# Kernel optimization log

Hardware: AMD Instinct MI355X
Metric: run time of the kernel (lower is better)

## Reference

```python
import jax, jax.numpy as jnp
import numpy as np

N, E, F_IN, HEADS, C_HEAD, HID, B, NCLS = 20000, 320000, 128, 2, 256, 512, 64, 38
EL = E + N  # edges with self-loops appended


def _bn(x, g, b, eps=1e-5):
    mu = jnp.mean(x, 0)
    var = jnp.mean((x - mu) ** 2, 0)
    return g * (x - mu) * jax.lax.rsqrt(var + eps) + b


def _gcn(x, W, b, src, dst):
    # src/dst already include self-loops; symmetric deg^-1/2 normalization (PyG GCNConv)
    h = x @ W                                             # [N, HID]
    deg = jax.ops.segment_sum(jnp.ones(EL, x.dtype), dst, N)
    norm = jax.lax.rsqrt(jnp.maximum(deg, 1.0))
    coef = norm[src] * norm[dst]                          # [EL]
    agg = jax.ops.segment_sum(h[src] * coef[:, None], dst, N)
    return agg + b


def _gat(x, W, a_src, a_dst, b, src, dst):
    # PyG GATConv, heads=2, concat: alpha = softmax_dst(leaky_relu(a_s.h_src + a_d.h_dst))
    h = (x @ W).reshape(N, HEADS, C_HEAD)
    as_n = jnp.sum(h * a_src, -1)                         # [N, HEADS]
    ad_n = jnp.sum(h * a_dst, -1)
    e = jax.nn.leaky_relu(as_n[src] + ad_n[dst], 0.2)     # [EL, HEADS]
    m = jax.ops.segment_max(e, dst, N)
    ex = jnp.exp(e - m[dst])
    s = jax.ops.segment_sum(ex, dst, N)
    alpha = ex / s[dst]                                   # [EL, HEADS]
    out = jax.ops.segment_sum(h[src] * alpha[:, :, None], dst, N)
    return out.reshape(N, HEADS * C_HEAD) + b


def setup_inputs() -> dict:
    key = jax.random.key(0)
    ks = jax.random.split(key, 40)
    x = jax.random.normal(ks[0], (N, F_IN), jnp.float32)
    edge_index = jax.random.randint(ks[1], (2, E), 0, N, jnp.int32)
    batch = jnp.sort(jax.random.randint(ks[2], (N,), 0, B, jnp.int32))

    def lin(k, fi, fo):
        bound = np.sqrt(6.0 / fi)
        return jax.random.uniform(k, (fi, fo), jnp.float32, -bound, bound)

    d = dict(x=x, edge_index=edge_index, batch=batch)
    # feature transform
    d['ft_W'] = lin(ks[3], F_IN, HID); d['ft_b'] = jnp.zeros(HID)
    d['ft_g'] = jnp.ones(HID); d['ft_be'] = jnp.zeros(HID)
    # GCN block
    d['gcn1_W'] = lin(ks[4], HID, HID); d['gcn1_b'] = jnp.zeros(HID)
    d['gbn1_g'] = jnp.ones(HID); d['gbn1_b'] = jnp.zeros(HID)
    d['gcn2_W'] = lin(ks[5], HID, HID); d['gcn2_b'] = jnp.zeros(HID)
    d['gbn2_g'] = jnp.ones(HID); d['gbn2_b'] = jnp.zeros(HID)
    # GAT block
    abound = np.sqrt(6.0 / HEADS)
    d['gat1_W'] = lin(ks[6], HID, HID)
    d['gat1_as'] = jax.random.uniform(ks[7], (HEADS, C_HEAD), jnp.float32, -abound, abound)
    d['gat1_ad'] = jax.random.uniform(ks[8], (HEADS, C_HEAD), jnp.float32, -abound, abound)
    d['gat1_b'] = jnp.zeros(HID)
    d['abn1_g'] = jnp.ones(HID); d['abn1_b'] = jnp.zeros(HID)
    d['gat2_W'] = lin(ks[9], HID, HID)
    d['gat2_as'] = jax.random.uniform(ks[10], (HEADS, C_HEAD), jnp.float32, -abound, abound)
    d['gat2_ad'] = jax.random.uniform(ks[11], (HEADS, C_HEAD), jnp.float32, -abound, abound)
    d['gat2_b'] = jnp.zeros(HID)
    d['abn2_g'] = jnp.ones(HID); d['abn2_b'] = jnp.zeros(HID)
    # classifier
    d['fc1_W'] = lin(ks[12], 2 * HID, HID); d['fc1_b'] = jnp.zeros(HID)
    d['cbn1_g'] = jnp.ones(HID); d['cbn1_b'] = jnp.zeros(HID)
    d['fc2_W'] = lin(ks[13], HID, HID // 2); d['fc2_b'] = jnp.zeros(HID // 2)
    d['cbn2_g'] = jnp.ones(HID // 2); d['cbn2_b'] = jnp.zeros(HID // 2)
    d['out_W'] = lin(ks[14], HID // 2, NCLS); d['out_b'] = jnp.zeros(NCLS)
    return d


def reference(x, edge_index, batch,
              ft_W, ft_b, ft_g, ft_be,
              gcn1_W, gcn1_b, gbn1_g, gbn1_b, gcn2_W, gcn2_b, gbn2_g, gbn2_b,
              gat1_W, gat1_as, gat1_ad, gat1_b, abn1_g, abn1_b,
              gat2_W, gat2_as, gat2_ad, gat2_b, abn2_g, abn2_b,
              fc1_W, fc1_b, cbn1_g, cbn1_b, fc2_W, fc2_b, cbn2_g, cbn2_b,
              out_W, out_b):
    loop = jnp.arange(N, dtype=edge_index.dtype)
    src = jnp.concatenate([edge_index[0], loop])
    dst = jnp.concatenate([edge_index[1], loop])

    # feature transform: Linear -> BN -> LeakyReLU(0.2)
    h = jax.nn.leaky_relu(_bn(x @ ft_W + ft_b, ft_g, ft_be), 0.2)
    # GCN block
    h = jax.nn.elu(_bn(_gcn(h, gcn1_W, gcn1_b, src, dst), gbn1_g, gbn1_b))
    h = jax.nn.elu(_bn(_gcn(h, gcn2_W, gcn2_b, src, dst), gbn2_g, gbn2_b))
    # GAT block
    h = jax.nn.elu(_bn(_gat(h, gat1_W, gat1_as, gat1_ad, gat1_b, src, dst), abn1_g, abn1_b))
    h = jax.nn.elu(_bn(_gat(h, gat2_W, gat2_as, gat2_ad, gat2_b, src, dst), abn2_g, abn2_b))
    # global mean+max pool over graphs
    cnt = jax.ops.segment_sum(jnp.ones(N, h.dtype), batch, B)
    mean_p = jax.ops.segment_sum(h, batch, B) / jnp.maximum(cnt, 1.0)[:, None]
    max_p = jax.ops.segment_max(h, batch, B)
    p = jnp.concatenate([mean_p, max_p], axis=1)           # [B, 1024]
    # classifier: fc1 -> bn -> fc2 -> bn -> leaky_relu -> out
    z = _bn(p @ fc1_W + fc1_b, cbn1_g, cbn1_b)
    z = _bn(z @ fc2_W + fc2_b, cbn2_g, cbn2_b)
    z = jax.nn.leaky_relu(z, 0.2)
    return z @ out_W + out_b                                # [B, NCLS]
```

## Files before the change

### kernel.cpp

```cpp
#include <hip/hip_runtime.h>

#define N_NODES 20000
#define N_EDGES 320000
#define EDG_ALL (N_EDGES + N_NODES)
#define F_IN 128
#define HID 512
#define NB 64
#define NCLS 38
#define M_PAD2 20480
#define ROW_BLKS 160
#define NBLK_SCAN ((N_NODES + 255) / 256)
#define BN_ROWS 16
#define BN_GRID ((N_NODES + BN_ROWS - 1) / BN_ROWS)
#define NPART 64
#define POOL_SPLIT 4

typedef short bf16x8 __attribute__((ext_vector_type(8)));
typedef float f32x4 __attribute__((ext_vector_type(4)));
typedef _Float16 f16;
typedef _Float16 f16x8 __attribute__((ext_vector_type(8)));

__device__ inline unsigned short f2bf(float f) {
  union { float f; unsigned u; } v; v.f = f;
  unsigned r = v.u + 0x7FFF + ((v.u >> 16) & 1);
  return (unsigned short)(r >> 16);
}

__device__ inline void split2(float f, unsigned short& h, unsigned short& l) {
  unsigned short hh = f2bf(f);
  union { unsigned u; float f; } vh; vh.u = ((unsigned)hh) << 16;
  h = hh;
  l = f2bf(f - vh.f);
}

__device__ inline void gload16(const void* g, void* l) {
  __builtin_amdgcn_global_load_lds(
      (const __attribute__((address_space(1))) unsigned int*)g,
      (__attribute__((address_space(3))) unsigned int*)l, 16, 0, 0);
}


__global__ void deg_count(const int* __restrict__ ei, int* __restrict__ deg) {
  int e = blockIdx.x * blockDim.x + threadIdx.x;
  if (e >= EDG_ALL) return;
  int d = (e < N_EDGES) ? ei[N_EDGES + e] : (e - N_EDGES);
  atomicAdd(&deg[d], 1);
}

__global__ void scan_p1(const int* __restrict__ deg, int* __restrict__ bsum) {
  __shared__ int sh[256];
  int b = blockIdx.x, t = threadIdx.x, i = b * 256 + t;
  sh[t] = (i < N_NODES) ? deg[i] : 0;
  __syncthreads();
  for (int o = 128; o > 0; o >>= 1) {
    if (t < o) sh[t] += sh[t + o];
    __syncthreads();
  }
  if (t == 0) bsum[b] = sh[0];
}

__global__ void scan_p2(const int* __restrict__ bsum, int* __restrict__ boff) {
  __shared__ int sh[128];
  int t = threadIdx.x;
  sh[t] = (t < NBLK_SCAN) ? bsum[t] : 0;
  __syncthreads();
  for (int o = 1; o < 128; o <<= 1) {
    int v = (t >= o) ? sh[t - o] : 0;
    __syncthreads();
    sh[t] += v;
    __syncthreads();
  }
  boff[t] = (t == 0) ? 0 : sh[t - 1];
}

__global__ void scan_p3(const int* __restrict__ deg, const int* __restrict__ boff,
                        int* __restrict__ row_ptr) {
  __shared__ int sh[256];
  int b = blockIdx.x, t = threadIdx.x, i = b * 256 + t;
  sh[t] = (i < N_NODES) ? deg[i] : 0;
  __syncthreads();
  for (int o = 1; o < 256; o <<= 1) {
    int v = (t >= o) ? sh[t - o] : 0;
    __syncthreads();
    sh[t] += v;
    __syncthreads();
  }
  if (i < N_NODES) row_ptr[i + 1] = boff[b] + sh[t];
  if (i == 0) row_ptr[0] = 0;
}

__global__ void compute_norm(const int* __restrict__ deg, float* __restrict__ norm) {
  int i = blockIdx.x * blockDim.x + threadIdx.x;
  if (i >= N_NODES) return;
  norm[i] = rsqrtf(fmaxf((float)deg[i], 1.f));
}

__global__ void fill_csr(const int* __restrict__ ei, int* __restrict__ cursor,
                         int* __restrict__ csr_src) {
  int e = blockIdx.x * blockDim.x + threadIdx.x;
  if (e >= EDG_ALL) return;
  int s, d;
  if (e < N_EDGES) { s = ei[e]; d = ei[N_EDGES + e]; }
  else { s = d = e - N_EDGES; }
  int pos = atomicAdd(&cursor[d], 1);
  csr_src[pos] = s;
}


__global__ void conv_split4(const float* __restrict__ in, unsigned short* __restrict__ hi,
                            unsigned short* __restrict__ lo, int n4) {
  int i = blockIdx.x * blockDim.x + threadIdx.x;
  if (i >= n4) return;
  float4 v = ((const float4*)in)[i];
  ushort4 h, l;
  split2(v.x, h.x, l.x); split2(v.y, h.y, l.y);
  split2(v.z, h.z, l.z); split2(v.w, h.w, l.w);
  ((ushort4*)hi)[i] = h;
  ((ushort4*)lo)[i] = l;
}

__global__ __launch_bounds__(256) void wtrans_split(const float* __restrict__ W,
                                                    unsigned short* __restrict__ WTh,
                                                    unsigned short* __restrict__ WTl,
                                                    int K, int N) {
  __shared__ float sh[32][33];
  int k0 = blockIdx.y * 32, n0 = blockIdx.x * 32;
  int r = threadIdx.x >> 5, c = threadIdx.x & 31;
#pragma unroll
  for (int i = 0; i < 4; ++i)
    sh[r + 8 * i][c] = W[(size_t)(k0 + r + 8 * i) * N + n0 + c];
  __syncthreads();
#pragma unroll
  for (int i = 0; i < 4; ++i) {
    unsigned short h, l;
    split2(sh[c][r + 8 * i], h, l);
    WTh[(size_t)(n0 + r + 8 * i) * K + k0 + c] = h;
    WTl[(size_t)(n0 + r + 8 * i) * K + k0 + c] = l;
  }
}

__global__ __launch_bounds__(256) void ftrans(const float* __restrict__ W,
                                              float* __restrict__ WT, int K, int N) {
  __shared__ float sh[32][33];
  int k0 = blockIdx.y * 32, n0 = blockIdx.x * 32;
  int r = threadIdx.x >> 5, c = threadIdx.x & 31;
#pragma unroll
  for (int i = 0; i < 4; ++i) {
    int k = k0 + r + 8 * i, n = n0 + c;
    sh[r + 8 * i][c] = (k < K && n < N) ? W[(size_t)k * N + n] : 0.f;
  }
  __syncthreads();
#pragma unroll
  for (int i = 0; i < 4; ++i) {
    int n = n0 + r + 8 * i, k = k0 + c;
    if (n < N && k < K) WT[(size_t)n * K + k] = sh[c][r + 8 * i];
  }
}


template <int K, typename OT>
__global__ __launch_bounds__(256) void mm_split(const unsigned short* __restrict__ Ah,
                                                const unsigned short* __restrict__ Al,
                                                const unsigned short* __restrict__ Bh,
                                                const unsigned short* __restrict__ Bl,
                                                const float* __restrict__ bias,
                                                OT* __restrict__ C) {
  __shared__ unsigned short AsH[4096], AsL[4096], BsH[4096], BsL[4096];
  const int t = threadIdx.x;
  const int wid = t >> 6, l = t & 63;
  const int bid = blockIdx.x;
  const int g = bid >> 5, w = bid & 31;
  const int row0 = (g * 8 + (w & 7)) * 128;
  const int col0 = (w >> 3) * 128;
  const int wm = wid >> 1, wn = wid & 1;

  f32x4 acc[4][4];
#pragma unroll
  for (int m = 0; m < 4; ++m)
#pragma unroll
    for (int n = 0; n < 4; ++n)
#pragma unroll
      for (int q = 0; q < 4; ++q) acc[m][n][q] = 0.f;

  const size_t aoff = (size_t)(row0 + wid * 32 + (l >> 2)) * K + (l & 3) * 8;
  const size_t boff = (size_t)(col0 + wid * 32 + (l >> 2)) * K + (l & 3) * 8;
  const unsigned short* gAh0 = Ah + aoff; const unsigned short* gAh1 = gAh0 + (size_t)16 * K;
  const unsigned short* gAl0 = Al + aoff; const unsigned short* gAl1 = gAl0 + (size_t)16 * K;
  const unsigned short* gBh0 = Bh + boff; const unsigned short* gBh1 = gBh0 + (size_t)16 * K;
  const unsigned short* gBl0 = Bl + boff; const unsigned short* gBl1 = gBl0 + (size_t)16 * K;
  unsigned short* lAh0 = &AsH[(wid * 2 + 0) * 512];
  unsigned short* lAh1 = &AsH[(wid * 2 + 1) * 512];
  unsigned short* lAl0 = &AsL[(wid * 2 + 0) * 512];
  unsigned short* lAl1 = &AsL[(wid * 2 + 1) * 512];
  unsigned short* lBh0 = &BsH[(wid * 2 + 0) * 512];
  unsigned short* lBh1 = &BsH[(wid * 2 + 1) * 512];
  unsigned short* lBl0 = &BsL[(wid * 2 + 0) * 512];
  unsigned short* lBl1 = &BsL[(wid * 2 + 1) * 512];

  const int lr = l & 15, kq = (l >> 4) * 8;

  for (int kt = 0; kt < K / 32; ++kt) {
    const int ko = kt * 32;
    gload16(gAh0 + ko, lAh0);
    gload16(gAh1 + ko, lAh1);
    gload16(gAl0 + ko, lAl0);
    gload16(gAl1 + ko, lAl1);
    gload16(gBh0 + ko, lBh0);
    gload16(gBh1 + ko, lBh1);
    gload16(gBl0 + ko, lBl0);
    gload16(gBl1 + ko, lBl1);
    __syncthreads();
    bf16x8 ah[4], al[4], bh[4], bl[4];
#pragma unroll
    for (int m = 0; m < 4; ++m) {
      int ro = (wm * 64 + m * 16 + lr) * 32 + kq;
      ah[m] = *(const bf16x8*)&AsH[ro];
      al[m] = *(const bf16x8*)&AsL[ro];
    }
#pragma unroll
    for (int n = 0; n < 4; ++n) {
      int ro = (wn * 64 + n * 16 + lr) * 32 + kq;
      bh[n] = *(const bf16x8*)&BsH[ro];
      bl[n] = *(const bf16x8*)&BsL[ro];
    }
#pragma unroll
    for (int m = 0; m < 4; ++m)
#pragma unroll
      for (int n = 0; n < 4; ++n) {
        acc[m][n] = __builtin_amdgcn_mfma_f32_16x16x32_bf16(ah[m], bh[n], acc[m][n], 0, 0, 0);
        acc[m][n] = __builtin_amdgcn_mfma_f32_16x16x32_bf16(al[m], bh[n], acc[m][n], 0, 0, 0);
        acc[m][n] = __builtin_amdgcn_mfma_f32_16x16x32_bf16(ah[m], bl[n], acc[m][n], 0, 0, 0);
      }
    __syncthreads();
  }

  const int lg = l >> 4;
#pragma unroll
  for (int m = 0; m < 4; ++m) {
    int row = row0 + wm * 64 + m * 16 + lg * 4;
#pragma unroll
    for (int n = 0; n < 4; ++n) {
      int col = col0 + wn * 64 + n * 16 + lr;
      float bv = bias ? bias[col] : 0.f;
#pragma unroll
      for (int j = 0; j < 4; ++j)
        C[(size_t)(row + j) * HID + col] = (OT)(acc[m][n][j] + bv);
    }
  }
}


__global__ __launch_bounds__(256) void colstats(const float* __restrict__ X, int n,
                                                float* __restrict__ part) {
  int t = threadIdx.x;
  int r0 = blockIdx.x * BN_ROWS;
  int r1 = min(r0 + BN_ROWS, n);
  float s0 = 0, q0 = 0, s1 = 0, q1 = 0;
  const float2* X2 = (const float2*)X;
  for (int r = r0; r < r1; ++r) {
    float2 v = X2[(size_t)r * 256 + t];
    s0 += v.x; q0 += v.x * v.x;
    s1 += v.y; q1 += v.y * v.y;
  }
  float* pb = part + (size_t)(blockIdx.x & (NPART - 1)) * 1024;
  atomicAdd(&pb[2 * t], s0);
  atomicAdd(&pb[2 * t + 1], s1);
  atomicAdd(&pb[HID + 2 * t], q0);
  atomicAdd(&pb[HID + 2 * t + 1], q1);
}

__global__ __launch_bounds__(256) void stats_comb(const float* __restrict__ part,
                                                  float* __restrict__ stats) {
  int j = blockIdx.x * 256 + threadIdx.x;
  float s = 0.f;
#pragma unroll 8
  for (int k = 0; k < NPART; ++k) s += part[(size_t)k * 1024 + j];
  stats[j] = s;
}

__global__ __launch_bounds__(256) void bn_act(float* __restrict__ X, int n,
                                              const float* __restrict__ stats,
                                              const float* __restrict__ g,
                                              const float* __restrict__ b, int act,
                                              unsigned short* __restrict__ hio,
                                              unsigned short* __restrict__ loo,
                                              int writeX) {
  int t = threadIdx.x;
  int r0 = blockIdx.x * BN_ROWS;
  int r1 = min(r0 + BN_ROWS, n);
  float invn = 1.f / (float)n;
  float mu0 = stats[2 * t] * invn, mu1 = stats[2 * t + 1] * invn;
  float v0 = stats[HID + 2 * t] * invn - mu0 * mu0;
  float v1 = stats[HID + 2 * t + 1] * invn - mu1 * mu1;
  float2 gg = ((const float2*)g)[t];
  float2 bb = ((const float2*)b)[t];
  float sc0 = gg.x * rsqrtf(v0 + 1e-5f);
  float sc1 = gg.y * rsqrtf(v1 + 1e-5f);
  float2* X2 = (float2*)X;
  ushort2* H2 = (ushort2*)hio;
  ushort2* L2p = (ushort2*)loo;
  for (int r = r0; r < r1; ++r) {
    float2 xv = X2[(size_t)r * 256 + t];
    float y0 = sc0 * (xv.x - mu0) + bb.x;
    float y1 = sc1 * (xv.y - mu1) + bb.y;
    if (act == 1) {
      y0 = y0 > 0.f ? y0 : 0.2f * y0;
      y1 = y1 > 0.f ? y1 : 0.2f * y1;
    } else {
      y0 = y0 > 0.f ? y0 : expm1f(y0);
      y1 = y1 > 0.f ? y1 : expm1f(y1);
    }
    unsigned short h0, l0, h1, l1;
    split2(y0, h0, l0);
    split2(y1, h1, l1);
    ushort2 hh; hh.x = h0; hh.y = h1;
    ushort2 ll; ll.x = l0; ll.y = l1;
    H2[(size_t)r * 256 + t] = hh;
    L2p[(size_t)r * 256 + t] = ll;
    if (writeX) {
      float2 yv; yv.x = y0; yv.y = y1;
      X2[(size_t)r * 256 + t] = yv;
    }
  }
}


__global__ __launch_bounds__(256) void gcn_agg_w(
    const f16* __restrict__ h, const int* __restrict__ row_ptr,
    const int* __restrict__ csr_src, const float* __restrict__ norm,
    const float* __restrict__ bias, float* __restrict__ out) {
  int node = blockIdx.x * 4 + (threadIdx.x >> 6);
  int l = threadIdx.x & 63;
  int beg = row_ptr[node], end = row_ptr[node + 1];
  float ni = norm[node];
  const f16x8* h8 = (const f16x8*)h;
  float acc[8] = {};
  int e = beg;
  for (; e + 4 <= end; e += 4) {
    int s0 = csr_src[e], s1 = csr_src[e + 1], s2 = csr_src[e + 2], s3 = csr_src[e + 3];
    float c0 = norm[s0] * ni, c1 = norm[s1] * ni, c2 = norm[s2] * ni, c3 = norm[s3] * ni;
    f16x8 v0 = h8[(size_t)s0 * 64 + l];
    f16x8 v1 = h8[(size_t)s1 * 64 + l];
    f16x8 v2 = h8[(size_t)s2 * 64 + l];
    f16x8 v3 = h8[(size_t)s3 * 64 + l];
#pragma unroll
    for (int k = 0; k < 8; ++k)
      acc[k] += c0 * (float)v0[k] + c1 * (float)v1[k] + c2 * (float)v2[k] + c3 * (float)v3[k];
  }
  for (; e < end; ++e) {
    int s = csr_src[e];
    float c = norm[s] * ni;
    f16x8 v = h8[(size_t)s * 64 + l];
#pragma unroll
    for (int k = 0; k < 8; ++k) acc[k] += c * (float)v[k];
  }
  float4 b0 = ((const float4*)bias)[l * 2];
  float4 b1 = ((const float4*)bias)[l * 2 + 1];
  float4 o0, o1;
  o0.x = acc[0] + b0.x; o0.y = acc[1] + b0.y; o0.z = acc[2] + b0.z; o0.w = acc[3] + b0.w;
  o1.x = acc[4] + b1.x; o1.y = acc[5] + b1.y; o1.z = acc[6] + b1.z; o1.w = acc[7] + b1.w;
  ((float4*)out)[(size_t)node * 128 + l * 2] = o0;
  ((float4*)out)[(size_t)node * 128 + l * 2 + 1] = o1;
}


__device__ inline float wave_sum(float v) {
#pragma unroll
  for (int o = 32; o > 0; o >>= 1) v += __shfl_down(v, o);
  return v;
}

typedef _Float16 f16x2 __attribute__((ext_vector_type(2)));
__global__ __launch_bounds__(256) void gat_prep_h(
    const f16* __restrict__ h, const float* __restrict__ a_src,
    const float* __restrict__ a_dst, float* __restrict__ asn, float* __restrict__ adn) {
  int i = blockIdx.x;
  int t = threadIdx.x;
  f16x2 hv = ((const f16x2*)h)[(size_t)i * 256 + t];
  float2 as2 = ((const float2*)a_src)[t];
  float2 ad2 = ((const float2*)a_dst)[t];
  float h0 = (float)hv.x, h1 = (float)hv.y;
  float s = h0 * as2.x + h1 * as2.y;
  float d = h0 * ad2.x + h1 * ad2.y;
  s = wave_sum(s); d = wave_sum(d);
  __shared__ float red[4][2];
  int w = t >> 6;
  if ((t & 63) == 0) { red[w][0] = s; red[w][1] = d; }
  __syncthreads();
  if (t == 0) {
    asn[2 * i]     = red[0][0] + red[1][0];
    asn[2 * i + 1] = red[2][0] + red[3][0];
    adn[2 * i]     = red[0][1] + red[1][1];
    adn[2 * i + 1] = red[2][1] + red[3][1];
  }
}

__device__ inline float lrelu(float v) { return v > 0.f ? v : 0.2f * v; }

__global__ __launch_bounds__(256) void gat_agg_w(
    const f16* __restrict__ h, const int* __restrict__ row_ptr,
    const int* __restrict__ csr_src, const float* __restrict__ asn,
    const float* __restrict__ adn, const float* __restrict__ bias,
    float* __restrict__ out) {
  int node = blockIdx.x * 4 + (threadIdx.x >> 6);
  int l = threadIdx.x & 63;
  int beg = row_ptr[node], end = row_ptr[node + 1];
  float ad0 = adn[2 * node], ad1 = adn[2 * node + 1];

  float m0 = -3.4e38f, m1 = -3.4e38f;
  for (int e = beg + l; e < end; e += 64) {
    int s = csr_src[e];
    m0 = fmaxf(m0, lrelu(asn[2 * s] + ad0));
    m1 = fmaxf(m1, lrelu(asn[2 * s + 1] + ad1));
  }
#pragma unroll
  for (int o = 32; o > 0; o >>= 1) {
    m0 = fmaxf(m0, __shfl_down(m0, o));
    m1 = fmaxf(m1, __shfl_down(m1, o));
  }
  float M0 = __shfl(m0, 0);
  float M1 = __shfl(m1, 0);

  const f16x8* h8 = (const f16x8*)h;
  float acc[8] = {};
  float sw0 = 0.f, sw1 = 0.f;
  int e = beg;
  for (; e + 4 <= end; e += 4) {
    int s0 = csr_src[e], s1 = csr_src[e + 1], s2 = csr_src[e + 2], s3 = csr_src[e + 3];
    float w00 = expf(lrelu(asn[2 * s0] + ad0) - M0), w01 = expf(lrelu(asn[2 * s0 + 1] + ad1) - M1);
    float w10 = expf(lrelu(asn[2 * s1] + ad0) - M0), w11 = expf(lrelu(asn[2 * s1 + 1] + ad1) - M1);
    float w20 = expf(lrelu(asn[2 * s2] + ad0) - M0), w21 = expf(lrelu(asn[2 * s2 + 1] + ad1) - M1);
    float w30 = expf(lrelu(asn[2 * s3] + ad0) - M0), w31 = expf(lrelu(asn[2 * s3 + 1] + ad1) - M1);
    sw0 += w00 + w10 + w20 + w30;
    sw1 += w01 + w11 + w21 + w31;
    f16x8 v0 = h8[(size_t)s0 * 64 + l];
    f16x8 v1 = h8[(size_t)s1 * 64 + l];
    f16x8 v2 = h8[(size_t)s2 * 64 + l];
    f16x8 v3 = h8[(size_t)s3 * 64 + l];
    float u0 = (l < 32) ? w00 : w01;
    float u1 = (l < 32) ? w10 : w11;
    float u2 = (l < 32) ? w20 : w21;
    float u3 = (l < 32) ? w30 : w31;
#pragma unroll
    for (int k = 0; k < 8; ++k)
      acc[k] += u0 * (float)v0[k] + u1 * (float)v1[k] + u2 * (float)v2[k] + u3 * (float)v3[k];
  }
  for (; e < end; ++e) {
    int s = csr_src[e];
    float w0 = expf(lrelu(asn[2 * s] + ad0) - M0);
    float w1 = expf(lrelu(asn[2 * s + 1] + ad1) - M1);
    sw0 += w0; sw1 += w1;
    f16x8 v = h8[(size_t)s * 64 + l];
    float u = (l < 32) ? w0 : w1;
#pragma unroll
    for (int k = 0; k < 8; ++k) acc[k] += u * (float)v[k];
  }
  float iS = (l < 32) ? (1.f / sw0) : (1.f / sw1);
  float4 b0 = ((const float4*)bias)[l * 2];
  float4 b1 = ((const float4*)bias)[l * 2 + 1];
  float4 o0, o1;
  o0.x = acc[0] * iS + b0.x; o0.y = acc[1] * iS + b0.y;
  o0.z = acc[2] * iS + b0.z; o0.w = acc[3] * iS + b0.w;
  o1.x = acc[4] * iS + b1.x; o1.y = acc[5] * iS + b1.y;
  o1.z = acc[6] * iS + b1.z; o1.w = acc[7] * iS + b1.w;
  ((float4*)out)[(size_t)node * 128 + l * 2] = o0;
  ((float4*)out)[(size_t)node * 128 + l * 2 + 1] = o1;
}


__global__ void graph_starts(const int* __restrict__ batch, int* __restrict__ start) {
  int i = blockIdx.x * blockDim.x + threadIdx.x;
  if (i >= N_NODES) return;
  int b = batch[i];
  int bp = (i == 0) ? -1 : batch[i - 1];
  for (int g = bp + 1; g <= b; ++g) start[g] = i;
  if (i == N_NODES - 1) {
    for (int g = b + 1; g <= NB; ++g) start[g] = N_NODES;
  }
}

__global__ __launch_bounds__(512) void pool_part(const float* __restrict__ h,
                                                 const int* __restrict__ start,
                                                 float* __restrict__ pp_sum,
                                                 float* __restrict__ pp_max) {
  int b = blockIdx.x, ch = blockIdx.y, t = threadIdx.x;
  int s = start[b], e = start[b + 1];
  int len = e - s;
  int c0 = s + (len * ch) / POOL_SPLIT;
  int c1 = s + (len * (ch + 1)) / POOL_SPLIT;
  float sum = 0.f, mx = -3.4e38f;
  int r = c0;
  for (; r + 4 <= c1; r += 4) {
    float v0 = h[(size_t)(r + 0) * HID + t];
    float v1 = h[(size_t)(r + 1) * HID + t];
    float v2 = h[(size_t)(r + 2) * HID + t];
    float v3 = h[(size_t)(r + 3) * HID + t];
    sum += v0 + v1 + v2 + v3;
    mx = fmaxf(mx, fmaxf(fmaxf(v0, v1), fmaxf(v2, v3)));
  }
  for (; r < c1; ++r) {
    float v = h[(size_t)r * HID + t];
    sum += v; mx = fmaxf(mx, v);
  }
  pp_sum[((size_t)b * POOL_SPLIT + ch) * HID + t] = sum;
  pp_max[((size_t)b * POOL_SPLIT + ch) * HID + t] = mx;
}

__global__ __launch_bounds__(512) void pool_comb(const float* __restrict__ pp_sum,
                                                 const float* __restrict__ pp_max,
                                                 const int* __restrict__ start,
                                                 float* __restrict__ p) {
  int b = blockIdx.x, t = threadIdx.x;
  float sum = 0.f, mx = -3.4e38f;
#pragma unroll
  for (int ch = 0; ch < POOL_SPLIT; ++ch) {
    sum += pp_sum[((size_t)b * POOL_SPLIT + ch) * HID + t];
    mx = fmaxf(mx, pp_max[((size_t)b * POOL_SPLIT + ch) * HID + t]);
  }
  float cnt = (float)(start[b + 1] - start[b]);
  p[b * 1024 + t] = sum / fmaxf(cnt, 1.f);
  p[b * 1024 + 512 + t] = mx;
}


__global__ __launch_bounds__(256) void fc_wave(const float* __restrict__ A,
                                               const float* __restrict__ WT,
                                               const float* __restrict__ bias,
                                               float* __restrict__ C, int K, int Ncol) {
  int r = blockIdx.x;
  int wid = threadIdx.x >> 6, l = threadIdx.x & 63;
  int c = blockIdx.y * 4 + wid;
  if (c >= Ncol) return;
  const float* a = A + (size_t)r * K;
  const float* w = WT + (size_t)c * K;
  float s = 0.f;
  for (int k = l; k < K; k += 64) s += a[k] * w[k];
#pragma unroll
  for (int o = 32; o > 0; o >>= 1) s += __shfl_down(s, o);
  if (l == 0) C[(size_t)r * Ncol + c] = s + bias[c];
}

__global__ void bn_small(float* __restrict__ X, int R, int C,
                         const float* __restrict__ g, const float* __restrict__ b, int act) {
  int c = blockIdx.x * blockDim.x + threadIdx.x;
  if (c >= C) return;
  float s = 0.f, q = 0.f;
  for (int r = 0; r < R; ++r) {
    float v = X[r * C + c];
    s += v; q += v * v;
  }
  float mu = s / R;
  float var = q / R - mu * mu;
  float sc = g[c] * rsqrtf(var + 1e-5f);
  float bb = b[c];
  for (int r = 0; r < R; ++r) {
    float v = sc * (X[r * C + c] - mu) + bb;
    if (act == 1) v = v > 0.f ? v : 0.2f * v;
    X[r * C + c] = v;
  }
}


extern "C" void kernel_launch(void* const* d_in, const int* in_sizes, int n_in,
                              void* d_out, int out_size, void* d_ws, size_t ws_size,
                              hipStream_t stream) {
  const float* x      = (const float*)d_in[0];
  const int*   ei     = (const int*)d_in[1];
  const int*   batch  = (const int*)d_in[2];
  const float* ft_W   = (const float*)d_in[3];
  const float* ft_b   = (const float*)d_in[4];
  const float* ft_g   = (const float*)d_in[5];
  const float* ft_be  = (const float*)d_in[6];
  const float* gcn1_W = (const float*)d_in[7];
  const float* gcn1_b = (const float*)d_in[8];
  const float* gbn1_g = (const float*)d_in[9];
  const float* gbn1_b = (const float*)d_in[10];
  const float* gcn2_W = (const float*)d_in[11];
  const float* gcn2_b = (const float*)d_in[12];
  const float* gbn2_g = (const float*)d_in[13];
  const float* gbn2_b = (const float*)d_in[14];
  const float* gat1_W = (const float*)d_in[15];
  const float* gat1_as= (const float*)d_in[16];
  const float* gat1_ad= (const float*)d_in[17];
  const float* gat1_b = (const float*)d_in[18];
  const float* abn1_g = (const float*)d_in[19];
  const float* abn1_b = (const float*)d_in[20];
  const float* gat2_W = (const float*)d_in[21];
  const float* gat2_as= (const float*)d_in[22];
  const float* gat2_ad= (const float*)d_in[23];
  const float* gat2_b = (const float*)d_in[24];
  const float* abn2_g = (const float*)d_in[25];
  const float* abn2_b = (const float*)d_in[26];
  const float* fc1_W  = (const float*)d_in[27];
  const float* fc1_b  = (const float*)d_in[28];
  const float* cbn1_g = (const float*)d_in[29];
  const float* cbn1_b = (const float*)d_in[30];
  const float* fc2_W  = (const float*)d_in[31];
  const float* fc2_b  = (const float*)d_in[32];
  const float* cbn2_g = (const float*)d_in[33];
  const float* cbn2_b = (const float*)d_in[34];
  const float* out_W  = (const float*)d_in[35];
  const float* out_b  = (const float*)d_in[36];

  char* ws = (char*)d_ws;
  size_t off = 0;
  auto alloc = [&](size_t bytes) -> void* {
    void* p = ws + off;
    off = (off + bytes + 255) & ~(size_t)255;
    return p;
  };

  float* buf0 = (float*)alloc((size_t)M_PAD2 * HID * 4);
  float* buf1 = (float*)alloc((size_t)M_PAD2 * HID * 4);
  unsigned short* ahi = (unsigned short*)alloc((size_t)M_PAD2 * HID * 2);
  unsigned short* alo = (unsigned short*)alloc((size_t)M_PAD2 * HID * 2);
  unsigned short* wh_ft = (unsigned short*)alloc((size_t)HID * F_IN * 2);
  unsigned short* wl_ft = (unsigned short*)alloc((size_t)HID * F_IN * 2);
  unsigned short* wh_g1 = (unsigned short*)alloc((size_t)HID * HID * 2);
  unsigned short* wl_g1 = (unsigned short*)alloc((size_t)HID * HID * 2);
  unsigned short* wh_g2 = (unsigned short*)alloc((size_t)HID * HID * 2);
  unsigned short* wl_g2 = (unsigned short*)alloc((size_t)HID * HID * 2);
  unsigned short* wh_a1 = (unsigned short*)alloc((size_t)HID * HID * 2);
  unsigned short* wl_a1 = (unsigned short*)alloc((size_t)HID * HID * 2);
  unsigned short* wh_a2 = (unsigned short*)alloc((size_t)HID * HID * 2);
  unsigned short* wl_a2 = (unsigned short*)alloc((size_t)HID * HID * 2);
  float* fc1t = (float*)alloc((size_t)512 * 1024 * 4);
  float* fc2t = (float*)alloc((size_t)256 * 512 * 4);
  float* outt = (float*)alloc((size_t)NCLS * 256 * 4);
  int*   row_ptr = (int*)alloc((N_NODES + 1) * 4);
  int*   cursor  = (int*)alloc(N_NODES * 4);
  int*   deg     = (int*)alloc(N_NODES * 4);
  int*   csr_src = (int*)alloc(EDG_ALL * 4);
  float* norm    = (float*)alloc(N_NODES * 4);
  float* asn     = (float*)alloc(N_NODES * 2 * 4);
  float* adn     = (float*)alloc(N_NODES * 2 * 4);
  float* stats   = (float*)alloc(1024 * 4);
  float* spart   = (float*)alloc((size_t)NPART * 1024 * 4);
  int*   bsum    = (int*)alloc(128 * 4);
  int*   boff    = (int*)alloc(128 * 4);
  int*   start   = (int*)alloc((NB + 1) * 4);
  float* p       = (float*)alloc(NB * 1024 * 4);
  float* pp_sum  = (float*)alloc((size_t)NB * POOL_SPLIT * HID * 4);
  float* pp_max  = (float*)alloc((size_t)NB * POOL_SPLIT * HID * 4);
  float* z1      = (float*)alloc(NB * HID * 4);
  float* z2      = (float*)alloc(NB * 256 * 4);
  unsigned short* xhi = (unsigned short*)buf0;
  unsigned short* xlo = xhi + (size_t)M_PAD2 * F_IN;
  f16* hbuf = (f16*)buf1;

  const dim3 blk256(256);
  const dim3 mmGrid(ROW_BLKS * 4);
  const int aggGrid = N_NODES / 4;

#define BN_BLOCK(XBUF, G, B, ACT, WX)                                            \
  hipMemsetAsync(spart, 0, (size_t)NPART * 1024 * 4, stream);                    \
  colstats<<<BN_GRID, blk256, 0, stream>>>(XBUF, N_NODES, spart);                \
  stats_comb<<<4, blk256, 0, stream>>>(spart, stats);                            \
  bn_act<<<BN_GRID, blk256, 0, stream>>>(XBUF, N_NODES, stats, G, B, ACT, ahi, alo, WX);

  hipMemsetAsync(deg, 0, N_NODES * 4, stream);
  deg_count<<<(EDG_ALL + 255) / 256, blk256, 0, stream>>>(ei, deg);
  scan_p1<<<NBLK_SCAN, blk256, 0, stream>>>(deg, bsum);
  scan_p2<<<1, 128, 0, stream>>>(bsum, boff);
  scan_p3<<<NBLK_SCAN, blk256, 0, stream>>>(deg, boff, row_ptr);
  compute_norm<<<(N_NODES + 255) / 256, blk256, 0, stream>>>(deg, norm);
  hipMemcpyAsync(cursor, row_ptr, N_NODES * 4, hipMemcpyDeviceToDevice, stream);
  fill_csr<<<(EDG_ALL + 255) / 256, blk256, 0, stream>>>(ei, cursor, csr_src);

  wtrans_split<<<dim3(HID / 32, F_IN / 32), blk256, 0, stream>>>(ft_W, wh_ft, wl_ft, F_IN, HID);
  wtrans_split<<<dim3(HID / 32, HID / 32), blk256, 0, stream>>>(gcn1_W, wh_g1, wl_g1, HID, HID);
  wtrans_split<<<dim3(HID / 32, HID / 32), blk256, 0, stream>>>(gcn2_W, wh_g2, wl_g2, HID, HID);
  wtrans_split<<<dim3(HID / 32, HID / 32), blk256, 0, stream>>>(gat1_W, wh_a1, wl_a1, HID, HID);
  wtrans_split<<<dim3(HID / 32, HID / 32), blk256, 0, stream>>>(gat2_W, wh_a2, wl_a2, HID, HID);
  ftrans<<<dim3(512 / 32, 1024 / 32), blk256, 0, stream>>>(fc1_W, fc1t, 1024, 512);
  ftrans<<<dim3(256 / 32, 512 / 32), blk256, 0, stream>>>(fc2_W, fc2t, 512, 256);
  ftrans<<<dim3((NCLS + 31) / 32, 256 / 32), blk256, 0, stream>>>(out_W, outt, 256, NCLS);

  conv_split4<<<(N_NODES * F_IN / 4 + 255) / 256, blk256, 0, stream>>>(x, xhi, xlo, N_NODES * F_IN / 4);
  mm_split<F_IN, float><<<mmGrid, blk256, 0, stream>>>(xhi, xlo, wh_ft, wl_ft, ft_b, buf1);
  BN_BLOCK(buf1, ft_g, ft_be, 1, 0)

  mm_split<HID, f16><<<mmGrid, blk256, 0, stream>>>(ahi, alo, wh_g1, wl_g1, nullptr, hbuf);
  gcn_agg_w<<<aggGrid, blk256, 0, stream>>>(hbuf, row_ptr, csr_src, norm, gcn1_b, buf0);
  BN_BLOCK(buf0, gbn1_g, gbn1_b, 2, 0)

  mm_split<HID, f16><<<mmGrid, blk256, 0, stream>>>(ahi, alo, wh_g2, wl_g2, nullptr, hbuf);
  gcn_agg_w<<<aggGrid, blk256, 0, stream>>>(hbuf, row_ptr, csr_src, norm, gcn2_b, buf0);
  BN_BLOCK(buf0, gbn2_g, gbn2_b, 2, 0)

  mm_split<HID, f16><<<mmGrid, blk256, 0, stream>>>(ahi, alo, wh_a1, wl_a1, nullptr, hbuf);
  gat_prep_h<<<N_NODES, blk256, 0, stream>>>(hbuf, gat1_as, gat1_ad, asn, adn);
  gat_agg_w<<<aggGrid, blk256, 0, stream>>>(hbuf, row_ptr, csr_src, asn, adn, gat1_b, buf0);
  BN_BLOCK(buf0, abn1_g, abn1_b, 2, 0)

  mm_split<HID, f16><<<mmGrid, blk256, 0, stream>>>(ahi, alo, wh_a2, wl_a2, nullptr, hbuf);
  gat_prep_h<<<N_NODES, blk256, 0, stream>>>(hbuf, gat2_as, gat2_ad, asn, adn);
  gat_agg_w<<<aggGrid, blk256, 0, stream>>>(hbuf, row_ptr, csr_src, asn, adn, gat2_b, buf0);
  BN_BLOCK(buf0, abn2_g, abn2_b, 2, 1)

  graph_starts<<<(N_NODES + 255) / 256, blk256, 0, stream>>>(batch, start);
  pool_part<<<dim3(NB, POOL_SPLIT), dim3(512), 0, stream>>>(buf0, start, pp_sum, pp_max);
  pool_comb<<<NB, dim3(512), 0, stream>>>(pp_sum, pp_max, start, p);

  fc_wave<<<dim3(NB, 128), blk256, 0, stream>>>(p, fc1t, fc1_b, z1, 1024, 512);
  bn_small<<<2, blk256, 0, stream>>>(z1, NB, 512, cbn1_g, cbn1_b, 0);
  fc_wave<<<dim3(NB, 64), blk256, 0, stream>>>(z1, fc2t, fc2_b, z2, 512, 256);
  bn_small<<<1, blk256, 0, stream>>>(z2, NB, 256, cbn2_g, cbn2_b, 1);
  fc_wave<<<dim3(NB, 10), blk256, 0, stream>>>(z2, outt, out_b, (float*)d_out, 256, NCLS);

#undef BN_BLOCK
  (void)in_sizes; (void)n_in; (void)out_size; (void)ws_size;
}
```

Baseline: 797.5 us.

## Replace atomic BN partials with per-block writes; precompute GAT max via edge-parallel atomics

The column-statistics kernel now writes one partial per block instead of atomically adding into 64 shared partial buffers. This removes the memset and the atomic contention, but the combine kernel now serially sums 1250 partials per column. The per-node softmax max in GAT aggregation is moved into a separate edge-parallel kernel that uses order-preserving unsigned atomicMax, which removes the first gather pass inside gat_agg_w. The trade-off is an extra memset, an extra launch and global atomics per GAT layer.

```diff
diff --git a/kernel.cpp b/kernel.cpp
--- a/kernel.cpp
+++ b/kernel.cpp
@@ -12,7 +12,6 @@
 #define NBLK_SCAN ((N_NODES + 255) / 256)
 #define BN_ROWS 16
 #define BN_GRID ((N_NODES + BN_ROWS - 1) / BN_ROWS)
-#define NPART 64
 #define POOL_SPLIT 4
 
 typedef short bf16x8 __attribute__((ext_vector_type(8)));
@@ -38,6 +37,17 @@
       (const __attribute__((address_space(1))) unsigned int*)g,
       (__attribute__((address_space(3))) unsigned int*)l, 16, 0, 0);
 }
+
+__device__ inline unsigned ordf(float x) {
+  unsigned u = __float_as_uint(x);
+  return (u & 0x80000000u) ? ~u : (u | 0x80000000u);
+}
+__device__ inline float deordf(unsigned v) {
+  unsigned u = (v & 0x80000000u) ? (v & 0x7FFFFFFFu) : ~v;
+  return __uint_as_float(u);
+}
+
+__device__ inline float lrelu(float v) { return v > 0.f ? v : 0.2f * v; }
 
 
 __global__ void deg_count(const int* __restrict__ ei, int* __restrict__ deg) {
@@ -262,19 +272,18 @@
     s0 += v.x; q0 += v.x * v.x;
     s1 += v.y; q1 += v.y * v.y;
   }
-  float* pb = part + (size_t)(blockIdx.x & (NPART - 1)) * 1024;
-  atomicAdd(&pb[2 * t], s0);
-  atomicAdd(&pb[2 * t + 1], s1);
-  atomicAdd(&pb[HID + 2 * t], q0);
-  atomicAdd(&pb[HID + 2 * t + 1], q1);
+  float* pb = part + (size_t)blockIdx.x * 1024;
+  pb[2 * t] = s0;
+  pb[2 * t + 1] = s1;
+  pb[HID + 2 * t] = q0;
+  pb[HID + 2 * t + 1] = q1;
 }
 
 __global__ __launch_bounds__(256) void stats_comb(const float* __restrict__ part,
                                                   float* __restrict__ stats) {
   int j = blockIdx.x * 256 + threadIdx.x;
   float s = 0.f;
-#pragma unroll 8
-  for (int k = 0; k < NPART; ++k) s += part[(size_t)k * 1024 + j];
+  for (int k = 0; k < BN_GRID; ++k) s += part[(size_t)k * 1024 + j];
   stats[j] = s;
 }
 
@@ -395,31 +404,30 @@
   }
 }
 
-__device__ inline float lrelu(float v) { return v > 0.f ? v : 0.2f * v; }
+__global__ void gat_max(const int* __restrict__ ei, const float* __restrict__ asn,
+                        const float* __restrict__ adn, unsigned* __restrict__ nmax) {
+  int e = blockIdx.x * blockDim.x + threadIdx.x;
+  if (e >= EDG_ALL) return;
+  int s, d;
+  if (e < N_EDGES) { s = ei[e]; d = ei[N_EDGES + e]; }
+  else { s = d = e - N_EDGES; }
+  float e0 = lrelu(asn[2 * s] + adn[2 * d]);
+  float e1 = lrelu(asn[2 * s + 1] + adn[2 * d + 1]);
+  atomicMax(&nmax[2 * d], ordf(e0));
+  atomicMax(&nmax[2 * d + 1], ordf(e1));
+}
 
 __global__ __launch_bounds__(256) void gat_agg_w(
     const f16* __restrict__ h, const int* __restrict__ row_ptr,
     const int* __restrict__ csr_src, const float* __restrict__ asn,
-    const float* __restrict__ adn, const float* __restrict__ bias,
-    float* __restrict__ out) {
+    const float* __restrict__ adn, const unsigned* __restrict__ nmax,
+    const float* __restrict__ bias, float* __restrict__ out) {
   int node = blockIdx.x * 4 + (threadIdx.x >> 6);
   int l = threadIdx.x & 63;
   int beg = row_ptr[node], end = row_ptr[node + 1];
   float ad0 = adn[2 * node], ad1 = adn[2 * node + 1];
-
-  float m0 = -3.4e38f, m1 = -3.4e38f;
-  for (int e = beg + l; e < end; e += 64) {
-    int s = csr_src[e];
-    m0 = fmaxf(m0, lrelu(asn[2 * s] + ad0));
-    m1 = fmaxf(m1, lrelu(asn[2 * s + 1] + ad1));
-  }
-#pragma unroll
-  for (int o = 32; o > 0; o >>= 1) {
-    m0 = fmaxf(m0, __shfl_down(m0, o));
-    m1 = fmaxf(m1, __shfl_down(m1, o));
-  }
-  float M0 = __shfl(m0, 0);
-  float M1 = __shfl(m1, 0);
+  float M0 = deordf(nmax[2 * node]);
+  float M1 = deordf(nmax[2 * node + 1]);
 
   const f16x8* h8 = (const f16x8*)h;
   float acc[8] = {};
@@ -634,8 +642,9 @@
   float* norm    = (float*)alloc(N_NODES * 4);
   float* asn     = (float*)alloc(N_NODES * 2 * 4);
   float* adn     = (float*)alloc(N_NODES * 2 * 4);
+  unsigned* nmax = (unsigned*)alloc(N_NODES * 2 * 4);
   float* stats   = (float*)alloc(1024 * 4);
-  float* spart   = (float*)alloc((size_t)NPART * 1024 * 4);
+  float* spart   = (float*)alloc((size_t)BN_GRID * 1024 * 4);
   int*   bsum    = (int*)alloc(128 * 4);
   int*   boff    = (int*)alloc(128 * 4);
   int*   start   = (int*)alloc((NB + 1) * 4);
@@ -653,7 +662,6 @@
   const int aggGrid = N_NODES / 4;
 
 #define BN_BLOCK(XBUF, G, B, ACT, WX)                                            \
-  hipMemsetAsync(spart, 0, (size_t)NPART * 1024 * 4, stream);                    \
   colstats<<<BN_GRID, blk256, 0, stream>>>(XBUF, N_NODES, spart);                \
   stats_comb<<<4, blk256, 0, stream>>>(spart, stats);                            \
   bn_act<<<BN_GRID, blk256, 0, stream>>>(XBUF, N_NODES, stats, G, B, ACT, ahi, alo, WX);
@@ -690,12 +698,16 @@
 
   mm_split<HID, f16><<<mmGrid, blk256, 0, stream>>>(ahi, alo, wh_a1, wl_a1, nullptr, hbuf);
   gat_prep_h<<<N_NODES, blk256, 0, stream>>>(hbuf, gat1_as, gat1_ad, asn, adn);
-  gat_agg_w<<<aggGrid, blk256, 0, stream>>>(hbuf, row_ptr, csr_src, asn, adn, gat1_b, buf0);
+  hipMemsetAsync(nmax, 0, N_NODES * 2 * 4, stream);
+  gat_max<<<(EDG_ALL + 255) / 256, blk256, 0, stream>>>(ei, asn, adn, nmax);
+  gat_agg_w<<<aggGrid, blk256, 0, stream>>>(hbuf, row_ptr, csr_src, asn, adn, nmax, gat1_b, buf0);
   BN_BLOCK(buf0, abn1_g, abn1_b, 2, 0)
 
   mm_split<HID, f16><<<mmGrid, blk256, 0, stream>>>(ahi, alo, wh_a2, wl_a2, nullptr, hbuf);
   gat_prep_h<<<N_NODES, blk256, 0, stream>>>(hbuf, gat2_as, gat2_ad, asn, adn);
-  gat_agg_w<<<aggGrid, blk256, 0, stream>>>(hbuf, row_ptr, csr_src, asn, adn, gat2_b, buf0);
+  hipMemsetAsync(nmax, 0, N_NODES * 2 * 4, stream);
+  gat_max<<<(EDG_ALL + 255) / 256, blk256, 0, stream>>>(ei, asn, adn, nmax);
+  gat_agg_w<<<aggGrid, blk256, 0, stream>>>(hbuf, row_ptr, csr_src, asn, adn, nmax, gat2_b, buf0);
   BN_BLOCK(buf0, abn2_g, abn2_b, 2, 1)
 
   graph_starts<<<(N_NODES + 255) / 256, blk256, 0, stream>>>(batch, start);
```

Measured after the change: 1.112 ms. +39.4%, slower.

## Store pre-BatchNorm activations in fp16 instead of fp32

Applied to the files above, without the earlier changes.

The matmul and aggregation outputs that feed BatchNorm, along with the final pooled activations, are now written and read as fp16 rather than fp32. This halves the traffic through colstats, bn_act, the aggregation epilogues and pool_part. pool_part is reworked to handle two columns per thread using 256-thread blocks. The cost is fp16 rounding and range limits on the pre-normalization values, which could hurt accuracy if those values are large.

```diff
diff --git a/kernel.cpp b/kernel.cpp
--- a/kernel.cpp
+++ b/kernel.cpp
@@ -18,6 +18,7 @@
 typedef short bf16x8 __attribute__((ext_vector_type(8)));
 typedef float f32x4 __attribute__((ext_vector_type(4)));
 typedef _Float16 f16;
+typedef _Float16 f16x2 __attribute__((ext_vector_type(2)));
 typedef _Float16 f16x8 __attribute__((ext_vector_type(8)));
 
 __device__ inline unsigned short f2bf(float f) {
@@ -38,6 +39,8 @@
       (const __attribute__((address_space(1))) unsigned int*)g,
       (__attribute__((address_space(3))) unsigned int*)l, 16, 0, 0);
 }
+
+__device__ inline float lrelu(float v) { return v > 0.f ? v : 0.2f * v; }
 
 
 __global__ void deg_count(const int* __restrict__ ei, int* __restrict__ deg) {
@@ -250,17 +253,18 @@
 }
 
 
-__global__ __launch_bounds__(256) void colstats(const float* __restrict__ X, int n,
+__global__ __launch_bounds__(256) void colstats(const f16* __restrict__ X, int n,
                                                 float* __restrict__ part) {
   int t = threadIdx.x;
   int r0 = blockIdx.x * BN_ROWS;
   int r1 = min(r0 + BN_ROWS, n);
   float s0 = 0, q0 = 0, s1 = 0, q1 = 0;
-  const float2* X2 = (const float2*)X;
+  const f16x2* X2 = (const f16x2*)X;
   for (int r = r0; r < r1; ++r) {
-    float2 v = X2[(size_t)r * 256 + t];
-    s0 += v.x; q0 += v.x * v.x;
-    s1 += v.y; q1 += v.y * v.y;
+    f16x2 v = X2[(size_t)r * 256 + t];
+    float a = (float)v.x, b = (float)v.y;
+    s0 += a; q0 += a * a;
+    s1 += b; q1 += b * b;
   }
   float* pb = part + (size_t)(blockIdx.x & (NPART - 1)) * 1024;
   atomicAdd(&pb[2 * t], s0);
@@ -278,7 +282,7 @@
   stats[j] = s;
 }
 
-__global__ __launch_bounds__(256) void bn_act(float* __restrict__ X, int n,
+__global__ __launch_bounds__(256) void bn_act(f16* __restrict__ X, int n,
                                               const float* __restrict__ stats,
                                               const float* __restrict__ g,
                                               const float* __restrict__ b, int act,
@@ -296,13 +300,13 @@
   float2 bb = ((const float2*)b)[t];
   float sc0 = gg.x * rsqrtf(v0 + 1e-5f);
   float sc1 = gg.y * rsqrtf(v1 + 1e-5f);
-  float2* X2 = (float2*)X;
+  f16x2* X2 = (f16x2*)X;
   ushort2* H2 = (ushort2*)hio;
   ushort2* L2p = (ushort2*)loo;
   for (int r = r0; r < r1; ++r) {
-    float2 xv = X2[(size_t)r * 256 + t];
-    float y0 = sc0 * (xv.x - mu0) + bb.x;
-    float y1 = sc1 * (xv.y - mu1) + bb.y;
+    f16x2 xv = X2[(size_t)r * 256 + t];
+    float y0 = sc0 * ((float)xv.x - mu0) + bb.x;
+    float y1 = sc1 * ((float)xv.y - mu1) + bb.y;
     if (act == 1) {
       y0 = y0 > 0.f ? y0 : 0.2f * y0;
       y1 = y1 > 0.f ? y1 : 0.2f * y1;
@@ -318,7 +322,7 @@
     H2[(size_t)r * 256 + t] = hh;
     L2p[(size_t)r * 256 + t] = ll;
     if (writeX) {
-      float2 yv; yv.x = y0; yv.y = y1;
+      f16x2 yv; yv.x = (f16)y0; yv.y = (f16)y1;
       X2[(size_t)r * 256 + t] = yv;
     }
   }
@@ -328,7 +332,7 @@
 __global__ __launch_bounds__(256) void gcn_agg_w(
     const f16* __restrict__ h, const int* __restrict__ row_ptr,
     const int* __restrict__ csr_src, const float* __restrict__ norm,
-    const float* __restrict__ bias, float* __restrict__ out) {
+    const float* __restrict__ bias, f16* __restrict__ out) {
   int node = blockIdx.x * 4 + (threadIdx.x >> 6);
   int l = threadIdx.x & 63;
   int beg = row_ptr[node], end = row_ptr[node + 1];
@@ -356,11 +360,12 @@
   }
   float4 b0 = ((const float4*)bias)[l * 2];
   float4 b1 = ((const float4*)bias)[l * 2 + 1];
-  float4 o0, o1;
-  o0.x = acc[0] + b0.x; o0.y = acc[1] + b0.y; o0.z = acc[2] + b0.z; o0.w = acc[3] + b0.w;
-  o1.x = acc[4] + b1.x; o1.y = acc[5] + b1.y; o1.z = acc[6] + b1.z; o1.w = acc[7] + b1.w;
-  ((float4*)out)[(size_t)node * 128 + l * 2] = o0;
-  ((float4*)out)[(size_t)node * 128 + l * 2 + 1] = o1;
+  f16x8 o;
+  o[0] = (f16)(acc[0] + b0.x); o[1] = (f16)(acc[1] + b0.y);
+  o[2] = (f16)(acc[2] + b0.z); o[3] = (f16)(acc[3] + b0.w);
+  o[4] = (f16)(acc[4] + b1.x); o[5] = (f16)(acc[5] + b1.y);
+  o[6] = (f16)(acc[6] + b1.z); o[7] = (f16)(acc[7] + b1.w);
+  ((f16x8*)out)[(size_t)node * 64 + l] = o;
 }
 
 
@@ -370,7 +375,6 @@
   return v;
 }
 
-typedef _Float16 f16x2 __attribute__((ext_vector_type(2)));
 __global__ __launch_bounds__(256) void gat_prep_h(
     const f16* __restrict__ h, const float* __restrict__ a_src,
     const float* __restrict__ a_dst, float* __restrict__ asn, float* __restrict__ adn) {
@@ -395,13 +399,11 @@
   }
 }
 
-__device__ inline float lrelu(float v) { return v > 0.f ? v : 0.2f * v; }
-
 __global__ __launch_bounds__(256) void gat_agg_w(
     const f16* __restrict__ h, const int* __restrict__ row_ptr,
     const int* __restrict__ csr_src, const float* __restrict__ asn,
     const float* __restrict__ adn, const float* __restrict__ bias,
-    float* __restrict__ out) {
+    f16* __restrict__ out) {
   int node = blockIdx.x * 4 + (threadIdx.x >> 6);
   int l = threadIdx.x & 63;
   int beg = row_ptr[node], end = row_ptr[node + 1];
@@ -458,13 +460,12 @@
   float iS = (l < 32) ? (1.f / sw0) : (1.f / sw1);
   float4 b0 = ((const float4*)bias)[l * 2];
   float4 b1 = ((const float4*)bias)[l * 2 + 1];
-  float4 o0, o1;
-  o0.x = acc[0] * iS + b0.x; o0.y = acc[1] * iS + b0.y;
-  o0.z = acc[2] * iS + b0.z; o0.w = acc[3] * iS + b0.w;
-  o1.x = acc[4] * iS + b1.x; o1.y = acc[5] * iS + b1.y;
-  o1.z = acc[6] * iS + b1.z; o1.w = acc[7] * iS + b1.w;
-  ((float4*)out)[(size_t)node * 128 + l * 2] = o0;
-  ((float4*)out)[(size_t)node * 128 + l * 2 + 1] = o1;
+  f16x8 o;
+  o[0] = (f16)(acc[0] * iS + b0.x); o[1] = (f16)(acc[1] * iS + b0.y);
+  o[2] = (f16)(acc[2] * iS + b0.z); o[3] = (f16)(acc[3] * iS + b0.w);
+  o[4] = (f16)(acc[4] * iS + b1.x); o[5] = (f16)(acc[5] * iS + b1.y);
+  o[6] = (f16)(acc[6] * iS + b1.z); o[7] = (f16)(acc[7] * iS + b1.w);
+  ((f16x8*)out)[(size_t)node * 64 + l] = o;
 }
 
 
@@ -479,7 +480,7 @@
   }
 }
 
-__global__ __launch_bounds__(512) void pool_part(const float* __restrict__ h,
+__global__ __launch_bounds__(256) void pool_part(const f16* __restrict__ h,
                                                  const int* __restrict__ start,
                                                  float* __restrict__ pp_sum,
                                                  float* __restrict__ pp_max) {
@@ -488,22 +489,28 @@
   int len = e - s;
   int c0 = s + (len * ch) / POOL_SPLIT;
   int c1 = s + (len * (ch + 1)) / POOL_SPLIT;
-  float sum = 0.f, mx = -3.4e38f;
+  const f16x2* h2 = (const f16x2*)h;
+  float s0 = 0.f, s1 = 0.f, m0 = -3.4e38f, m1 = -3.4e38f;
   int r = c0;
-  for (; r + 4 <= c1; r += 4) {
-    float v0 = h[(size_t)(r + 0) * HID + t];
-    float v1 = h[(size_t)(r + 1) * HID + t];
-    float v2 = h[(size_t)(r + 2) * HID + t];
-    float v3 = h[(size_t)(r + 3) * HID + t];
-    sum += v0 + v1 + v2 + v3;
-    mx = fmaxf(mx, fmaxf(fmaxf(v0, v1), fmaxf(v2, v3)));
+  for (; r + 2 <= c1; r += 2) {
+    f16x2 v0 = h2[(size_t)(r + 0) * 256 + t];
+    f16x2 v1 = h2[(size_t)(r + 1) * 256 + t];
+    float a0 = (float)v0.x, a1 = (float)v0.y, b0 = (float)v1.x, b1 = (float)v1.y;
+    s0 += a0 + b0; s1 += a1 + b1;
+    m0 = fmaxf(m0, fmaxf(a0, b0));
+    m1 = fmaxf(m1, fmaxf(a1, b1));
   }
   for (; r < c1; ++r) {
-    float v = h[(size_t)r * HID + t];
-    sum += v; mx = fmaxf(mx, v);
-  }
-  pp_sum[((size_t)b * POOL_SPLIT + ch) * HID + t] = sum;
-  pp_max[((size_t)b * POOL_SPLIT + ch) * HID + t] = mx;
+    f16x2 v = h2[(size_t)r * 256 + t];
+    float a0 = (float)v.x, a1 = (float)v.y;
+    s0 += a0; s1 += a1;
+    m0 = fmaxf(m0, a0); m1 = fmaxf(m1, a1);
+  }
+  size_t base = ((size_t)b * POOL_SPLIT + ch) * HID;
+  pp_sum[base + 2 * t] = s0;
+  pp_sum[base + 2 * t + 1] = s1;
+  pp_max[base + 2 * t] = m0;
+  pp_max[base + 2 * t + 1] = m1;
 }
 
 __global__ __launch_bounds__(512) void pool_comb(const float* __restrict__ pp_sum,
@@ -646,6 +653,7 @@
   float* z2      = (float*)alloc(NB * 256 * 4);
   unsigned short* xhi = (unsigned short*)buf0;
   unsigned short* xlo = xhi + (size_t)M_PAD2 * F_IN;
+  f16* xbuf = (f16*)buf0;
   f16* hbuf = (f16*)buf1;
 
   const dim3 blk256(256);
@@ -677,29 +685,29 @@
   ftrans<<<dim3((NCLS + 31) / 32, 256 / 32), blk256, 0, stream>>>(out_W, outt, 256, NCLS);
 
   conv_split4<<<(N_NODES * F_IN / 4 + 255) / 256, blk256, 0, stream>>>(x, xhi, xlo, N_NODES * F_IN / 4);
-  mm_split<F_IN, float><<<mmGrid, blk256, 0, stream>>>(xhi, xlo, wh_ft, wl_ft, ft_b, buf1);
-  BN_BLOCK(buf1, ft_g, ft_be, 1, 0)
+  mm_split<F_IN, f16><<<mmGrid, blk256, 0, stream>>>(xhi, xlo, wh_ft, wl_ft, ft_b, hbuf);
+  BN_BLOCK(hbuf, ft_g, ft_be, 1, 0)
 
   mm_split<HID, f16><<<mmGrid, blk256, 0, stream>>>(ahi, alo, wh_g1, wl_g1, nullptr, hbuf);
-  gcn_agg_w<<<aggGrid, blk256, 0, stream>>>(hbuf, row_ptr, csr_src, norm, gcn1_b, buf0);
-  BN_BLOCK(buf0, gbn1_g, gbn1_b, 2, 0)
+  gcn_agg_w<<<aggGrid, blk256, 0, stream>>>(hbuf, row_ptr, csr_src, norm, gcn1_b, xbuf);
+  BN_BLOCK(xbuf, gbn1_g, gbn1_b, 2, 0)
 
   mm_split<HID, f16><<<mmGrid, blk256, 0, stream>>>(ahi, alo, wh_g2, wl_g2, nullptr, hbuf);
-  gcn_agg_w<<<aggGrid, blk256, 0, stream>>>(hbuf, row_ptr, csr_src, norm, gcn2_b, buf0);
-  BN_BLOCK(buf0, gbn2_g, gbn2_b, 2, 0)
+  gcn_agg_w<<<aggGrid, blk256, 0, stream>>>(hbuf, row_ptr, csr_src, norm, gcn2_b, xbuf);
+  BN_BLOCK(xbuf, gbn2_g, gbn2_b, 2, 0)
 
   mm_split<HID, f16><<<mmGrid, blk256, 0, stream>>>(ahi, alo, wh_a1, wl_a1, nullptr, hbuf);
   gat_prep_h<<<N_NODES, blk256, 0, stream>>>(hbuf, gat1_as, gat1_ad, asn, adn);
-  gat_agg_w<<<aggGrid, blk256, 0, stream>>>(hbuf, row_ptr, csr_src, asn, adn, gat1_b, buf0);
-  BN_BLOCK(buf0, abn1_g, abn1_b, 2, 0)
+  gat_agg_w<<<aggGrid, blk256, 0, stream>>>(hbuf, row_ptr, csr_src, asn, adn, gat1_b, xbuf);
+  BN_BLOCK(xbuf, abn1_g, abn1_b, 2, 0)
 
   mm_split<HID, f16><<<mmGrid, blk256, 0, stream>>>(ahi, alo, wh_a2, wl_a2, nullptr, hbuf);
   gat_prep_h<<<N_NODES, blk256, 0, stream>>>(hbuf, gat2_as, gat2_ad, asn, adn);
-  gat_agg_w<<<aggGrid, blk256, 0, stream>>>(hbuf, row_ptr, csr_src, asn, adn, gat2_b, buf0);
-  BN_BLOCK(buf0, abn2_g, abn2_b, 2, 1)
+  gat_agg_w<<<aggGrid, blk256, 0, stream>>>(hbuf, row_ptr, csr_src, asn, adn, gat2_b, xbuf);
+  BN_BLOCK(xbuf, abn2_g, abn2_b, 2, 1)
 
   graph_starts<<<(N_NODES + 255) / 256, blk256, 0, stream>>>(batch, start);
-  pool_part<<<dim3(NB, POOL_SPLIT), dim3(512), 0, stream>>>(buf0, start, pp_sum, pp_max);
+  pool_part<<<dim3(NB, POOL_SPLIT), blk256, 0, stream>>>(xbuf, start, pp_sum, pp_max);
   pool_comb<<<NB, dim3(512), 0, stream>>>(pp_sum, pp_max, start, p);
 
   fc_wave<<<dim3(NB, 128), blk256, 0, stream>>>(p, fc1t, fc1_b, z1, 1024, 512);
```

Result: no change. 785.5 us (-1.5%).
